# Kernel tuning notes

Hardware: AMD Instinct MI355X
Metric: run time of the kernel (lower is better)

The kernel has to match this reference:

```python
import jax, jax.numpy as jnp
import numpy as np

B, S, D, H = 2, 4096, 512, 4
HD = D // H          # head_dim = key_size = value_size = 128
BLK = 512            # mask_block_size (tri-block-diagonal mask)


def setup_inputs() -> dict:
    key = jax.random.key(0)
    ks = jax.random.split(key, 7)
    # tri-block-diagonal boolean mask: query block attends to itself and adjacent blocks
    blk = np.arange(S) // BLK
    mask = np.abs(blk[:, None] - blk[None, :]) <= 1
    w_scale = 1.0 / np.sqrt(D)  # ~ variance_scaling fan_in init magnitude
    return {
        "q_input": jax.random.normal(ks[0], (B, S, D), jnp.float32),
        "kv_input": jax.random.normal(ks[1], (B, S, D), jnp.float32),
        "Wq": jax.random.normal(ks[2], (D, H * HD), jnp.float32) * w_scale,
        "Wk": jax.random.normal(ks[3], (D, H * HD), jnp.float32) * w_scale,
        "Wv": jax.random.normal(ks[4], (D, H * HD), jnp.float32) * w_scale,
        "Wo": jax.random.normal(ks[5], (H * HD, D), jnp.float32) * w_scale,
        "bo": jnp.zeros((D,), jnp.float32),
        "mask": jnp.asarray(mask),
    }


def reference(q_input, kv_input, Wq, Wk, Wv, Wo, bo, mask):
    b, s, _ = q_input.shape
    # multihead projections -> [b, s, H, HD]
    q = (q_input @ Wq).reshape(b, s, H, HD)
    k = (kv_input @ Wk).reshape(b, s, H, HD)
    v = (kv_input @ Wv).reshape(b, s, H, HD)
    # normalize_q=True: scale by key_size**-0.5 (no tanh soft cap)
    q = q * (HD ** -0.5)
    # masked attention (splash attention math): [b, H, sq, sk]
    scores = jnp.einsum("bqhd,bkhd->bhqk", q, k)
    neg = jnp.finfo(scores.dtype).min
    scores = jnp.where(mask[None, None], scores, neg)
    p = jax.nn.softmax(scores, axis=-1)
    out = jnp.einsum("bhqk,bkhd->bqhd", p, v)
    out = out.reshape(b, s, H * HD)
    return out @ Wo + bo
```

## Files before the change

kernel.cpp:

```cpp
#include <hip/hip_runtime.h>
#include <hip/hip_bf16.h>

#define S_LEN 4096
#define D_MODEL 512
#define NHEADS 4
#define HEAD_DIM 128
#define BATCH 2
#define M_ROWS 8192

typedef unsigned short u16;
typedef __attribute__((ext_vector_type(8))) short bf16x8;
typedef __attribute__((ext_vector_type(4))) short bf16x4;
typedef __attribute__((ext_vector_type(4))) float f32x4;

__device__ __forceinline__ float bf2f(u16 u) {
    return __uint_as_float(((unsigned)u) << 16);
}
__device__ __forceinline__ short f2b(float f) {
    unsigned x = __float_as_uint(f);
    unsigned r = (x + 0x7fffu + ((x >> 16) & 1u)) >> 16;
    return (short)r;
}

__device__ __forceinline__ int detect_f32(const u16* u, int nelem, int tid, int* s_cnt) {
    if (tid == 0) *s_cnt = 0;
    __syncthreads();
    int samp = nelem < 4096 ? nelem : 4096;
    int c = 0;
    for (int i = tid; i < samp; i += 256) {
        float af = fabsf(bf2f(u[i]));
        if (af != 0.0f && (!(af <= 1e12f) || af < 1e-12f)) c++;
    }
    atomicAdd(s_cnt, c);
    __syncthreads();
    return *s_cnt > 16;
}

__global__ __launch_bounds__(256) void prep_all(const void* qin, const void* kvin,
                                                const void* w0, const void* w1,
                                                const void* w2, const void* w3,
                                                u16* qa, u16* kva, u16* wt) {
    __shared__ int s_cnt;
    __shared__ float tile[32][33];
    const int tid = threadIdx.x, bid = blockIdx.x;
    if (bid < 2048) {
        const int which = bid >> 10, chunk = bid & 1023;
        const void* src = which ? kvin : qin;
        u16* dst = which ? kva : qa;
        const int f32 = detect_f32((const u16*)src, 4194304, tid, &s_cnt);
        const size_t base = (size_t)chunk * 4096 + (size_t)tid * 16;
        if (f32) {
            const float* s = (const float*)src + base;
            short v[16];
#pragma unroll
            for (int i = 0; i < 4; i++) {
                f32x4 t = *(const f32x4*)(s + 4 * i);
                v[4 * i] = f2b(t.x); v[4 * i + 1] = f2b(t.y);
                v[4 * i + 2] = f2b(t.z); v[4 * i + 3] = f2b(t.w);
            }
            *(bf16x8*)(dst + base) = *(bf16x8*)v;
            *(bf16x8*)(dst + base + 8) = *(bf16x8*)(v + 8);
        } else {
            const u16* s = (const u16*)src + base;
            *(bf16x8*)(dst + base) = *(const bf16x8*)s;
            *(bf16x8*)(dst + base + 8) = *(const bf16x8*)(s + 8);
        }
    } else {
        const int idx = bid - 2048, wi = idx >> 8, t = idx & 255;
        const void* W = (wi == 0) ? w0 : (wi == 1) ? w1 : (wi == 2) ? w2 : w3;
        const int f32 = detect_f32((const u16*)W, 262144, tid, &s_cnt);
        const float scale = (wi == 0) ? 0.0883883476483184f : 1.0f;
        u16* Wt = wt + (size_t)wi * D_MODEL * D_MODEL;
        const int k0 = (t >> 4) * 32, n0 = (t & 15) * 32;
        const int tx = tid & 31, ty = tid >> 5;
#pragma unroll
        for (int i = 0; i < 4; i++) {
            int r = ty + 8 * i;
            long long off = (long long)(k0 + r) * D_MODEL + n0 + tx;
            float v = f32 ? ((const float*)W)[off] : bf2f(((const u16*)W)[off]);
            tile[r][tx] = v * scale;
        }
        __syncthreads();
#pragma unroll
        for (int i = 0; i < 4; i++) {
            int r = ty + 8 * i;
            Wt[(size_t)(n0 + r) * D_MODEL + k0 + tx] = (u16)f2b(tile[tx][r]);
        }
    }
}

__global__ __launch_bounds__(256) void proj_mfma(const u16* qa, const u16* kva,
                                                 const u16* wt, u16* qb, u16* kb,
                                                 u16* vbT) {
    __shared__ short As[64][72];
    __shared__ short Ws[128][72];
    const int z = blockIdx.z;
    const u16* A = (z == 0) ? qa : kva;
    const u16* Wt = wt + (size_t)z * 262144;
    const int row0 = blockIdx.x * 64, col0 = blockIdx.y * 128;
    const int tid = threadIdx.x;
    const int lane = tid & 63, wid = tid >> 6;
    const int wm = wid >> 1, wn = wid & 1;
    const int l16 = lane & 15, quad = lane >> 4;
    const int ar = tid >> 2, ak = (tid & 3) * 16;
    const int wr = tid >> 1, wk = (tid & 1) * 32;

    f32x4 acc[2][4];
#pragma unroll
    for (int i = 0; i < 2; i++)
#pragma unroll
        for (int j = 0; j < 4; j++) acc[i][j] = (f32x4){0.f, 0.f, 0.f, 0.f};

    for (int k0 = 0; k0 < D_MODEL; k0 += 64) {
        {
            const u16* ap = A + (size_t)(row0 + ar) * D_MODEL + k0 + ak;
            *(bf16x8*)&As[ar][ak] = *(const bf16x8*)ap;
            *(bf16x8*)&As[ar][ak + 8] = *(const bf16x8*)(ap + 8);
            const u16* wp = Wt + (size_t)(col0 + wr) * D_MODEL + k0 + wk;
#pragma unroll
            for (int i = 0; i < 4; i++)
                *(bf16x8*)&Ws[wr][wk + 8 * i] = *(const bf16x8*)(wp + 8 * i);
        }
        __syncthreads();
#pragma unroll
        for (int kc = 0; kc < 2; kc++) {
            bf16x8 af[2], bfr[4];
#pragma unroll
            for (int i = 0; i < 2; i++)
                af[i] = *(const bf16x8*)&As[wm * 32 + i * 16 + l16][kc * 32 + quad * 8];
#pragma unroll
            for (int j = 0; j < 4; j++)
                bfr[j] = *(const bf16x8*)&Ws[wn * 64 + j * 16 + l16][kc * 32 + quad * 8];
#pragma unroll
            for (int i = 0; i < 2; i++)
#pragma unroll
                for (int j = 0; j < 4; j++)
                    acc[i][j] = __builtin_amdgcn_mfma_f32_16x16x32_bf16(af[i], bfr[j],
                                                                       acc[i][j], 0, 0, 0);
        }
        __syncthreads();
    }
    if (z == 2) {
#pragma unroll
        for (int i = 0; i < 2; i++) {
            int grow = row0 + wm * 32 + i * 16 + quad * 4;
            int b = grow >> 12, s = grow & (S_LEN - 1);
#pragma unroll
            for (int j = 0; j < 4; j++) {
                int gcol = col0 + wn * 64 + j * 16 + l16;
                int h = gcol >> 7, d = gcol & 127;
                short v[4];
#pragma unroll
                for (int r = 0; r < 4; r++) v[r] = f2b(acc[i][j][r]);
                *(bf16x4*)&vbT[((size_t)(b * NHEADS + h) * HEAD_DIM + d) * S_LEN + s] =
                    *(bf16x4*)v;
            }
        }
    } else {
        u16* out = (z == 0) ? qb : kb;
#pragma unroll
        for (int i = 0; i < 2; i++) {
            int grow = row0 + wm * 32 + i * 16 + quad * 4;
#pragma unroll
            for (int j = 0; j < 4; j++) {
                int gcol = col0 + wn * 64 + j * 16 + l16;
                int h = gcol >> 7, d = gcol & 127;
#pragma unroll
                for (int r = 0; r < 4; r++) {
                    int row = grow + r;
                    int b = row >> 12, s = row & (S_LEN - 1);
                    out[((size_t)(b * NHEADS + h) * S_LEN + s) * HEAD_DIM + d] =
                        (u16)f2b(acc[i][j][r]);
                }
            }
        }
    }
}

__global__ __launch_bounds__(256, 3) void attn_mfma(const u16* qb, const u16* kb,
                                                    const u16* vbT, u16* op0, u16* op1,
                                                    u16* op2, float* lp) {
    __shared__ short Ks[32][136];
    __shared__ short Vs[128][40];
    __shared__ short Ps[128][40];
    const int bid = blockIdx.x;
    const int bh = bid & 7;
    const int rest = bid >> 3;
    const int qt = rest / 3;
    const int p3 = rest - qt * 3;
    const int q0 = qt << 7;
    const int qblk = q0 >> 9;
    const int kstart0 = (qblk == 0) ? 0 : ((qblk - 1) << 9);
    const int kend0 = (qblk == 7) ? S_LEN : ((qblk + 2) << 9);
    const int kcount = kend0 - kstart0;
    const int third = (kcount / 3) & ~31;
    const int rem32 = (kcount - 3 * third) >> 5;
    const int kstart = kstart0 + p3 * third + (p3 < rem32 ? p3 : rem32) * 32;
    const int klen = third + (p3 < rem32 ? 32 : 0);
    const int tid = threadIdx.x;
    const int lane = tid & 63, wid = tid >> 6;
    const int l16 = lane & 15, quad = lane >> 4;
    const u16* qp = qb + (size_t)bh * S_LEN * HEAD_DIM;
    const u16* kp = kb + (size_t)bh * S_LEN * HEAD_DIM;
    const u16* vp = vbT + (size_t)bh * HEAD_DIM * S_LEN;

    bf16x8 qf[2][4];
    {
        const int r = tid >> 3, c0 = (tid & 7) * 16;
        for (int c = 0; c < 4; c++) {
            const u16* src = qp + (size_t)(q0 + c * 32 + r) * HEAD_DIM + c0;
            *(bf16x8*)&Ks[r][c0] = *(const bf16x8*)src;
            *(bf16x8*)&Ks[r][c0 + 8] = *(const bf16x8*)(src + 8);
            __syncthreads();
            if (wid == c) {
#pragma unroll
                for (int i = 0; i < 2; i++)
#pragma unroll
                    for (int kc = 0; kc < 4; kc++)
                        qf[i][kc] = *(const bf16x8*)&Ks[i * 16 + l16][kc * 32 + quad * 8];
            }
            __syncthreads();
        }
    }

    f32x4 o[2][8], lacc[2];
#pragma unroll
    for (int i = 0; i < 2; i++) {
        lacc[i] = (f32x4){0.f, 0.f, 0.f, 0.f};
#pragma unroll
        for (int n = 0; n < 8; n++) o[i][n] = (f32x4){0.f, 0.f, 0.f, 0.f};
    }
    bf16x8 ones;
#pragma unroll
    for (int t = 0; t < 8; t++) ones[t] = (short)0x3F80;

    for (int kk = 0; kk < klen; kk += 32) {
        const int kt = kstart + kk;
        {
            int r = tid >> 3, c0 = (tid & 7) * 16;
            const u16* src = kp + (size_t)(kt + r) * HEAD_DIM + c0;
            *(bf16x8*)&Ks[r][c0] = *(const bf16x8*)src;
            *(bf16x8*)&Ks[r][c0 + 8] = *(const bf16x8*)(src + 8);
        }
        {
            int d = tid >> 1, c0 = (tid & 1) * 16;
            const u16* src = vp + (size_t)d * S_LEN + kt + c0;
            *(bf16x8*)&Vs[d][c0] = *(const bf16x8*)src;
            *(bf16x8*)&Vs[d][c0 + 8] = *(const bf16x8*)(src + 8);
        }
        __syncthreads();
        f32x4 sa[2][2];
#pragma unroll
        for (int ki = 0; ki < 2; ki++)
#pragma unroll
            for (int qi = 0; qi < 2; qi++) sa[ki][qi] = (f32x4){0.f, 0.f, 0.f, 0.f};
#pragma unroll
        for (int kc = 0; kc < 4; kc++) {
            bf16x8 kf0 = *(const bf16x8*)&Ks[l16][kc * 32 + quad * 8];
            bf16x8 kf1 = *(const bf16x8*)&Ks[16 + l16][kc * 32 + quad * 8];
#pragma unroll
            for (int qi = 0; qi < 2; qi++) {
                sa[0][qi] = __builtin_amdgcn_mfma_f32_16x16x32_bf16(kf0, qf[qi][kc], sa[0][qi], 0, 0, 0);
                sa[1][qi] = __builtin_amdgcn_mfma_f32_16x16x32_bf16(kf1, qf[qi][kc], sa[1][qi], 0, 0, 0);
            }
        }
#pragma unroll
        for (int ki = 0; ki < 2; ki++) {
#pragma unroll
            for (int qi = 0; qi < 2; qi++) {
                short pv[4];
#pragma unroll
                for (int r = 0; r < 4; r++)
                    pv[r] = f2b(__expf(sa[ki][qi][r] - 8.0f));
                *(bf16x4*)&Ps[wid * 32 + qi * 16 + l16][ki * 16 + quad * 4] = *(bf16x4*)pv;
            }
        }
        __syncthreads();
        bf16x8 pf[2];
#pragma unroll
        for (int i = 0; i < 2; i++) {
            pf[i] = *(const bf16x8*)&Ps[wid * 32 + i * 16 + l16][quad * 8];
            lacc[i] = __builtin_amdgcn_mfma_f32_16x16x32_bf16(pf[i], ones, lacc[i], 0, 0, 0);
        }
#pragma unroll
        for (int n = 0; n < 8; n++) {
            bf16x8 vf = *(const bf16x8*)&Vs[n * 16 + l16][quad * 8];
#pragma unroll
            for (int i = 0; i < 2; i++)
                o[i][n] = __builtin_amdgcn_mfma_f32_16x16x32_bf16(pf[i], vf, o[i][n], 0, 0, 0);
        }
        __syncthreads();
    }
    u16* op = (p3 == 0) ? op0 : (p3 == 1 ? op1 : op2);
#pragma unroll
    for (int i = 0; i < 2; i++) {
#pragma unroll
        for (int r = 0; r < 4; r++) {
            int row = wid * 32 + i * 16 + quad * 4 + r;
            size_t gq = (size_t)bh * S_LEN + q0 + row;
#pragma unroll
            for (int n = 0; n < 8; n++)
                op[gq * HEAD_DIM + n * 16 + l16] = (u16)f2b(o[i][n][r]);
            if (l16 == 0) lp[(size_t)p3 * 8 * S_LEN + gq] = lacc[i][r];
        }
    }
}

__global__ __launch_bounds__(256) void outproj_mfma(const u16* op0, const u16* op1,
                                                    const u16* op2, const float* lp,
                                                    const u16* Wt, const void* bias,
                                                    float* out) {
    __shared__ int s_cnt;
    __shared__ short As[64][72];
    __shared__ short Ws[128][72];
    const int tid = threadIdx.x;
    const int f32b = detect_f32((const u16*)bias, 512, tid, &s_cnt);
    const int row0 = blockIdx.x * 64, col0 = blockIdx.y * 128;
    const int lane = tid & 63, wid = tid >> 6;
    const int wm = wid >> 1, wn = wid & 1;
    const int l16 = lane & 15, quad = lane >> 4;
    const int sr = tid >> 2, sk = (tid & 3) * 16;
    const int wr = tid >> 1, wk = (tid & 1) * 32;
    const size_t N = (size_t)8 * S_LEN;
    const int arow = row0 + sr;
    const int ab = arow >> 12, as = arow & (S_LEN - 1);
    f32x4 acc[2][4];
#pragma unroll
    for (int i = 0; i < 2; i++)
#pragma unroll
        for (int j = 0; j < 4; j++) acc[i][j] = (f32x4){0.f, 0.f, 0.f, 0.f};

    for (int k0 = 0; k0 < D_MODEL; k0 += 64) {
        {
            const int h = (k0 + sk) >> 7, d = (k0 + sk) & 127;
            const size_t gq = (size_t)(ab * NHEADS + h) * S_LEN + as;
            float inv = 1.0f / (lp[gq] + lp[N + gq] + lp[2 * N + gq]);
            const size_t base = gq * HEAD_DIM + d;
            bf16x8 a0 = *(const bf16x8*)&op0[base];
            bf16x8 a1 = *(const bf16x8*)&op1[base];
            bf16x8 a2 = *(const bf16x8*)&op2[base];
            bf16x8 b0 = *(const bf16x8*)&op0[base + 8];
            bf16x8 b1 = *(const bf16x8*)&op1[base + 8];
            bf16x8 b2 = *(const bf16x8*)&op2[base + 8];
            short v[16];
#pragma unroll
            for (int i = 0; i < 8; i++) {
                v[i] = f2b((bf2f((u16)a0[i]) + bf2f((u16)a1[i]) + bf2f((u16)a2[i])) * inv);
                v[8 + i] = f2b((bf2f((u16)b0[i]) + bf2f((u16)b1[i]) + bf2f((u16)b2[i])) * inv);
            }
            *(bf16x8*)&As[sr][sk] = *(bf16x8*)v;
            *(bf16x8*)&As[sr][sk + 8] = *(bf16x8*)(v + 8);
        }
        {
            const u16* wp = Wt + (size_t)(col0 + wr) * D_MODEL + k0 + wk;
#pragma unroll
            for (int i = 0; i < 4; i++)
                *(bf16x8*)&Ws[wr][wk + 8 * i] = *(const bf16x8*)(wp + 8 * i);
        }
        __syncthreads();
#pragma unroll
        for (int kc = 0; kc < 2; kc++) {
            bf16x8 af[2], bfr[4];
#pragma unroll
            for (int i = 0; i < 2; i++)
                af[i] = *(const bf16x8*)&As[wm * 32 + i * 16 + l16][kc * 32 + quad * 8];
#pragma unroll
            for (int j = 0; j < 4; j++)
                bfr[j] = *(const bf16x8*)&Ws[wn * 64 + j * 16 + l16][kc * 32 + quad * 8];
#pragma unroll
            for (int i = 0; i < 2; i++)
#pragma unroll
                for (int j = 0; j < 4; j++)
                    acc[i][j] = __builtin_amdgcn_mfma_f32_16x16x32_bf16(af[i], bfr[j],
                                                                       acc[i][j], 0, 0, 0);
        }
        __syncthreads();
    }
#pragma unroll
    for (int i = 0; i < 2; i++) {
        int grow = row0 + wm * 32 + i * 16 + quad * 4;
#pragma unroll
        for (int j = 0; j < 4; j++) {
            int gcol = col0 + wn * 64 + j * 16 + l16;
            float bval = f32b ? ((const float*)bias)[gcol] : bf2f(((const u16*)bias)[gcol]);
#pragma unroll
            for (int r = 0; r < 4; r++)
                out[(size_t)(grow + r) * D_MODEL + gcol] = acc[i][j][r] + bval;
        }
    }
}

extern "C" void kernel_launch(void* const* d_in, const int* in_sizes, int n_in,
                              void* d_out, int out_size, void* d_ws, size_t ws_size,
                              hipStream_t stream) {
    (void)in_sizes; (void)out_size; (void)ws_size; (void)n_in;
    const void* q_input = d_in[0];
    const void* kv_input = d_in[1];
    const void* Wq = d_in[2];
    const void* Wk = d_in[3];
    const void* Wv = d_in[4];
    const void* Wo = d_in[5];
    const void* bo = d_in[6];

    const size_t NELEM = (size_t)M_ROWS * D_MODEL;
    u16* wt = (u16*)d_ws;
    u16* qa = wt + 4 * 262144;
    u16* kva = qa + NELEM;
    u16* qb = kva + NELEM;
    u16* kb = qb + NELEM;
    u16* vbT = kb + NELEM;
    u16* op2 = vbT + NELEM;
    float* lp = (float*)(op2 + NELEM);
    u16* op0 = qa;
    u16* op1 = kva;

    prep_all<<<3072, 256, 0, stream>>>(q_input, kv_input, Wq, Wk, Wv, Wo, qa, kva, wt);
    proj_mfma<<<dim3(128, 4, 3), 256, 0, stream>>>(qa, kva, wt, qb, kb, vbT);
    attn_mfma<<<8 * 32 * 3, 256, 0, stream>>>(qb, kb, vbT, op0, op1, op2, lp);
    outproj_mfma<<<dim3(128, 4), 256, 0, stream>>>(op0, op1, op2, lp, wt + 3 * 262144,
                                                   bo, (float*)d_out);
}
```

Measured before the change: 217.0 us.

## Double-buffer K/V tiles via direct global-to-LDS loads with swizzled layout

Replaces the register-staged K/V (and Q) shared-memory loads in the attention kernel with `global_load_lds` transfers into a double-buffered, XOR-swizzled LDS layout. The next tile's loads are issued before the current tile's compute, and two of the three barriers per iteration are removed. This is meant to overlap memory latency with MFMA work and cut bank conflicts and sync stalls. It also packs the bf16 conversion of P with `v_cvt_pk_bf16_f32` and raises wave priority around the MFMA blocks via `s_setprio`, at the cost of more LDS per block and reliance on per-wave ownership of the P rows.

```diff
diff --git a/kernel.cpp b/kernel.cpp
--- a/kernel.cpp
+++ b/kernel.cpp
@@ -20,6 +20,18 @@
     unsigned x = __float_as_uint(f);
     unsigned r = (x + 0x7fffu + ((x >> 16) & 1u)) >> 16;
     return (short)r;
+}
+
+__device__ __forceinline__ unsigned cvtpk_bf16(float lo, float hi) {
+    unsigned r;
+    asm("v_cvt_pk_bf16_f32 %0, %1, %2" : "=v"(r) : "v"(lo), "v"(hi));
+    return r;
+}
+
+typedef __attribute__((address_space(1))) const unsigned int g_u32;
+typedef __attribute__((address_space(3))) unsigned int l_u32;
+__device__ __forceinline__ void gload16(const u16* g, short* l) {
+    __builtin_amdgcn_global_load_lds((g_u32*)g, (l_u32*)l, 16, 0, 0);
 }
 
 __device__ __forceinline__ int detect_f32(const u16* u, int nelem, int tid, int* s_cnt) {
@@ -180,8 +192,7 @@
 __global__ __launch_bounds__(256, 3) void attn_mfma(const u16* qb, const u16* kb,
                                                     const u16* vbT, u16* op0, u16* op1,
                                                     u16* op2, float* lp) {
-    __shared__ short Ks[32][136];
-    __shared__ short Vs[128][40];
+    __shared__ short SM[2][8192];
     __shared__ short Ps[128][40];
     const int bid = blockIdx.x;
     const int bh = bid & 7;
@@ -203,24 +214,38 @@
     const u16* qp = qb + (size_t)bh * S_LEN * HEAD_DIM;
     const u16* kp = kb + (size_t)bh * S_LEN * HEAD_DIM;
     const u16* vp = vbT + (size_t)bh * HEAD_DIM * S_LEN;
+    short* smf = &SM[0][0];
+
+    size_t koff[2], voff[2];
+    int sdst[2];
+#pragma unroll
+    for (int s = 0; s < 2; s++) {
+        const int wc = wid * 2 + s;
+        const int kr = wc * 4 + quad;
+        koff[s] = (size_t)kr * HEAD_DIM + (size_t)((l16 ^ (kr & 7)) * 8);
+        const int vr = wc * 16 + (lane >> 2);
+        voff[s] = (size_t)vr * S_LEN + (size_t)(((lane & 3) ^ (vr & 3)) * 8);
+        sdst[s] = wc * 512;
+    }
 
     bf16x8 qf[2][4];
     {
-        const int r = tid >> 3, c0 = (tid & 7) * 16;
-        for (int c = 0; c < 4; c++) {
-            const u16* src = qp + (size_t)(q0 + c * 32 + r) * HEAD_DIM + c0;
-            *(bf16x8*)&Ks[r][c0] = *(const bf16x8*)src;
-            *(bf16x8*)&Ks[r][c0 + 8] = *(const bf16x8*)(src + 8);
-            __syncthreads();
-            if (wid == c) {
-#pragma unroll
-                for (int i = 0; i < 2; i++)
-#pragma unroll
-                    for (int kc = 0; kc < 4; kc++)
-                        qf[i][kc] = *(const bf16x8*)&Ks[i * 16 + l16][kc * 32 + quad * 8];
-            }
-            __syncthreads();
-        }
+#pragma unroll
+        for (int c = 0; c < 4; c++)
+#pragma unroll
+            for (int s = 0; s < 2; s++)
+                gload16(qp + (size_t)(q0 + c * 32) * HEAD_DIM + koff[s],
+                        smf + c * 4096 + sdst[s]);
+        __syncthreads();
+#pragma unroll
+        for (int i = 0; i < 2; i++)
+#pragma unroll
+            for (int kc = 0; kc < 4; kc++) {
+                const int row = i * 16 + l16;
+                const int ch = (kc * 4 + quad) ^ (row & 7);
+                qf[i][kc] = *(const bf16x8*)&smf[wid * 4096 + row * 128 + ch * 8];
+            }
+        __syncthreads();
     }
 
     f32x4 o[2][8], lacc[2];
@@ -234,62 +259,80 @@
 #pragma unroll
     for (int t = 0; t < 8; t++) ones[t] = (short)0x3F80;
 
-    for (int kk = 0; kk < klen; kk += 32) {
-        const int kt = kstart + kk;
-        {
-            int r = tid >> 3, c0 = (tid & 7) * 16;
-            const u16* src = kp + (size_t)(kt + r) * HEAD_DIM + c0;
-            *(bf16x8*)&Ks[r][c0] = *(const bf16x8*)src;
-            *(bf16x8*)&Ks[r][c0 + 8] = *(const bf16x8*)(src + 8);
-        }
-        {
-            int d = tid >> 1, c0 = (tid & 1) * 16;
-            const u16* src = vp + (size_t)d * S_LEN + kt + c0;
-            *(bf16x8*)&Vs[d][c0] = *(const bf16x8*)src;
-            *(bf16x8*)&Vs[d][c0 + 8] = *(const bf16x8*)(src + 8);
-        }
-        __syncthreads();
+    {
+        const u16* kt_p = kp + (size_t)kstart * HEAD_DIM;
+        const u16* vt_p = vp + kstart;
+#pragma unroll
+        for (int s = 0; s < 2; s++) {
+            gload16(kt_p + koff[s], smf + sdst[s]);
+            gload16(vt_p + voff[s], smf + 4096 + sdst[s]);
+        }
+    }
+    const int nt = klen >> 5;
+    for (int t = 0; t < nt; t++) {
+        const int b = t & 1;
+        const short* kbuf = smf + b * 8192;
+        const short* vbuf = kbuf + 4096;
+        __syncthreads();
+        if (t + 1 < nt) {
+            const int kt = kstart + (t + 1) * 32;
+            const u16* kt_p = kp + (size_t)kt * HEAD_DIM;
+            const u16* vt_p = vp + kt;
+            short* dbuf = smf + (b ^ 1) * 8192;
+#pragma unroll
+            for (int s = 0; s < 2; s++) {
+                gload16(kt_p + koff[s], dbuf + sdst[s]);
+                gload16(vt_p + voff[s], dbuf + 4096 + sdst[s]);
+            }
+        }
         f32x4 sa[2][2];
 #pragma unroll
         for (int ki = 0; ki < 2; ki++)
 #pragma unroll
             for (int qi = 0; qi < 2; qi++) sa[ki][qi] = (f32x4){0.f, 0.f, 0.f, 0.f};
+        __builtin_amdgcn_s_setprio(1);
 #pragma unroll
         for (int kc = 0; kc < 4; kc++) {
-            bf16x8 kf0 = *(const bf16x8*)&Ks[l16][kc * 32 + quad * 8];
-            bf16x8 kf1 = *(const bf16x8*)&Ks[16 + l16][kc * 32 + quad * 8];
+            const int ch = ((kc * 4 + quad) ^ (l16 & 7)) * 8;
+            bf16x8 kf0 = *(const bf16x8*)&kbuf[l16 * 128 + ch];
+            bf16x8 kf1 = *(const bf16x8*)&kbuf[(16 + l16) * 128 + ch];
 #pragma unroll
             for (int qi = 0; qi < 2; qi++) {
                 sa[0][qi] = __builtin_amdgcn_mfma_f32_16x16x32_bf16(kf0, qf[qi][kc], sa[0][qi], 0, 0, 0);
                 sa[1][qi] = __builtin_amdgcn_mfma_f32_16x16x32_bf16(kf1, qf[qi][kc], sa[1][qi], 0, 0, 0);
             }
         }
+        __builtin_amdgcn_s_setprio(0);
 #pragma unroll
         for (int ki = 0; ki < 2; ki++) {
 #pragma unroll
             for (int qi = 0; qi < 2; qi++) {
-                short pv[4];
-#pragma unroll
-                for (int r = 0; r < 4; r++)
-                    pv[r] = f2b(__expf(sa[ki][qi][r] - 8.0f));
-                *(bf16x4*)&Ps[wid * 32 + qi * 16 + l16][ki * 16 + quad * 4] = *(bf16x4*)pv;
-            }
-        }
-        __syncthreads();
+                const float e0 = __expf(sa[ki][qi][0] - 8.0f);
+                const float e1 = __expf(sa[ki][qi][1] - 8.0f);
+                const float e2 = __expf(sa[ki][qi][2] - 8.0f);
+                const float e3 = __expf(sa[ki][qi][3] - 8.0f);
+                uint2 pk;
+                pk.x = cvtpk_bf16(e0, e1);
+                pk.y = cvtpk_bf16(e2, e3);
+                *(uint2*)&Ps[wid * 32 + qi * 16 + l16][ki * 16 + quad * 4] = pk;
+            }
+        }
         bf16x8 pf[2];
 #pragma unroll
         for (int i = 0; i < 2; i++) {
             pf[i] = *(const bf16x8*)&Ps[wid * 32 + i * 16 + l16][quad * 8];
             lacc[i] = __builtin_amdgcn_mfma_f32_16x16x32_bf16(pf[i], ones, lacc[i], 0, 0, 0);
         }
+        __builtin_amdgcn_s_setprio(1);
 #pragma unroll
         for (int n = 0; n < 8; n++) {
-            bf16x8 vf = *(const bf16x8*)&Vs[n * 16 + l16][quad * 8];
+            const int d = n * 16 + l16;
+            bf16x8 vf = *(const bf16x8*)&vbuf[d * 32 + ((quad ^ (d & 3)) * 8)];
 #pragma unroll
             for (int i = 0; i < 2; i++)
                 o[i][n] = __builtin_amdgcn_mfma_f32_16x16x32_bf16(pf[i], vf, o[i][n], 0, 0, 0);
         }
-        __syncthreads();
+        __builtin_amdgcn_s_setprio(0);
     }
     u16* op = (p3 == 0) ? op0 : (p3 == 1 ? op1 : op2);
 #pragma unroll
```

Result: faster. 211.3 us (-2.6%).
